# Optimization experiments

Hardware: AMD Instinct MI355X
Metric: run time of the kernel (lower is better)

The kernel has to match this reference:

```python
import jax, jax.numpy as jnp
import numpy as np

N, D, H, C, E = 16384, 768, 768, 2, 20

def setup_inputs() -> dict:
    key = jax.random.key(0)
    k1, k2, k3, k4, k5, k6 = jax.random.split(key, 6)
    return {
        "embeddings": jax.random.normal(k1, (N, D), dtype=jnp.float32),
        "component_idx": jax.random.randint(k2, (N,), 0, E, dtype=jnp.int64),
        "W1": jax.random.normal(k3, (E, D, H), dtype=jnp.float32) * (1.0 / np.sqrt(D)),
        "b1": jnp.zeros((E, H), dtype=jnp.float32),
        "W2": jax.random.normal(k4, (E, H, C), dtype=jnp.float32) * (1.0 / np.sqrt(H)),
        "b2": jnp.zeros((E, C), dtype=jnp.float32),
    }

def reference(embeddings, component_idx, W1, b1, W2, b2):
    # Each token n goes through expert component_idx[n]:
    #   y = relu(x @ W1[e] + b1[e]) @ W2[e] + b2[e]
    # The torch module's mask/cat/argsort reassembly is mathematically a
    # per-token select of its own expert's output at the original position.
    # Dense-expert formulation (standard jax MoE fallback), then gather.
    h = jax.nn.relu(jnp.einsum('nd,edh->enh', embeddings, W1) + b1[:, None, :])  # [E,N,H]
    y = jnp.einsum('enh,ehc->enc', h, W2) + b2[:, None, :]                        # [E,N,C]
    n_idx = jnp.arange(embeddings.shape[0])
    return y[component_idx, n_idx]  # [N,C]
```

## Files before the change

### kernel.cpp

```cpp
#include <hip/hip_runtime.h>

#define N_D 768
#define N_H 768
#define N_C 2
#define N_E 20
#define MT 128
#define NT 128
#define BK 32
#define KT (N_D / BK)
#define ROWB (N_D * 2)
#define SLOTMAX 160

typedef __attribute__((ext_vector_type(8))) short short8;
typedef __attribute__((ext_vector_type(4))) float f32x4;

__device__ __forceinline__ unsigned short f2bf(float f) {
  unsigned u = __builtin_bit_cast(unsigned, f);
  u += 0x7FFFu + ((u >> 16) & 1u);
  return (unsigned short)(u >> 16);
}

#define GLD_LDS16(gp, lp)                                                        \
  __builtin_amdgcn_global_load_lds(                                              \
      (const __attribute__((address_space(1))) void*)(gp),                       \
      (__attribute__((address_space(3))) void*)(lp), 16, 0, 0)


__global__ __launch_bounds__(256) void k_hist(const int* __restrict__ cidx,
                                              int* __restrict__ counts, int n) {
  __shared__ int lc[N_E];
  if (threadIdx.x < N_E) lc[threadIdx.x] = 0;
  __syncthreads();
  for (int i = blockIdx.x * blockDim.x + threadIdx.x; i < n;
       i += gridDim.x * blockDim.x) {
    int e = cidx[i];
    e = e < 0 ? 0 : (e >= N_E ? N_E - 1 : e);
    atomicAdd(&lc[e], 1);
  }
  __syncthreads();
  if (threadIdx.x < N_E) atomicAdd(&counts[threadIdx.x], lc[threadIdx.x]);
}

__global__ __launch_bounds__(64) void k_scan(const int* __restrict__ counts,
                                             int* __restrict__ offsets,
                                             int* __restrict__ cursor,
                                             int* __restrict__ slots) {
  int t = threadIdx.x;
  if (t < N_E) {
    int run = 0;
    for (int e = 0; e < t; ++e) run += counts[e];
    offsets[t] = run;
    cursor[t] = run;
  }
  if (t < 8) {
    int idx = 0;
    for (int e = t; e < N_E; e += 8) {
      int nt = (counts[e] + MT - 1) / MT;
      for (int m = 0; m < nt; ++m)
        for (int bx = 0; bx < 6; ++bx)
          if (idx < SLOTMAX) slots[t * SLOTMAX + idx++] = e | (m << 8) | (bx << 16);
    }
    for (; idx < SLOTMAX; ++idx) slots[t * SLOTMAX + idx] = -1;
  }
}

__global__ __launch_bounds__(256) void k_scatter(const int* __restrict__ cidx,
                                                 int* __restrict__ cursor,
                                                 int* __restrict__ sorted, int n) {
  __shared__ int lc[N_E];
  __shared__ int lbase[N_E];
  int tid = threadIdx.x;
  if (tid < N_E) lc[tid] = 0;
  __syncthreads();
  int i = blockIdx.x * blockDim.x + tid;
  int e = 0, p = 0;
  if (i < n) {
    e = cidx[i];
    e = e < 0 ? 0 : (e >= N_E ? N_E - 1 : e);
    p = atomicAdd(&lc[e], 1);
  }
  __syncthreads();
  if (tid < N_E) lbase[tid] = atomicAdd(&cursor[tid], lc[tid]);
  __syncthreads();
  if (i < n) sorted[lbase[e] + p] = i;
}


__global__ __launch_bounds__(192) void k_gather(const float* __restrict__ emb,
                                                const int* __restrict__ sorted,
                                                unsigned short* __restrict__ Xg,
                                                int n) {
  int row = blockIdx.x;
  int j = threadIdx.x;
  ushort4 o;
  if (row < n) {
    float4 v = ((const float4*)(emb + (size_t)sorted[row] * N_D))[j];
    o.x = f2bf(v.x);
    o.y = f2bf(v.y);
    o.z = f2bf(v.z);
    o.w = f2bf(v.w);
  } else {
    o.x = o.y = o.z = o.w = 0;
  }
  ((ushort4*)(Xg + (size_t)row * N_D))[j] = o;
}


__global__ __launch_bounds__(256) void k_w1_cvt(const float* __restrict__ W1,
                                                unsigned short* __restrict__ W1t) {
  __shared__ float tile[64][65];
  int e = blockIdx.z, h0 = blockIdx.x * 64, d0 = blockIdx.y * 64;
  const float* src = W1 + (size_t)e * N_D * N_H;
  unsigned short* dst = W1t + (size_t)e * N_H * N_D;
  int tx = threadIdx.x & 15, ty = threadIdx.x >> 4;
  for (int s = 0; s < 4; ++s) {
    int d = s * 16 + ty;
    float4 v = *(const float4*)&src[(size_t)(d0 + d) * N_H + h0 + tx * 4];
    tile[d][tx * 4 + 0] = v.x;
    tile[d][tx * 4 + 1] = v.y;
    tile[d][tx * 4 + 2] = v.z;
    tile[d][tx * 4 + 3] = v.w;
  }
  __syncthreads();
  int px = threadIdx.x & 7, py = threadIdx.x >> 3;
  for (int s = 0; s < 2; ++s) {
    int h = s * 32 + py;
    short8 v;
    for (int j = 0; j < 8; ++j)
      v[j] = (short)f2bf(tile[px * 8 + j][h]);
    *(short8*)&dst[(size_t)(h0 + h) * N_D + d0 + px * 8] = v;
  }
}


__global__ __launch_bounds__(256, 4) void k_gemm(
    const unsigned short* __restrict__ Xg, const unsigned short* __restrict__ W1t,
    const float* __restrict__ b1, const float* __restrict__ W2,
    const float* __restrict__ b2, const int* __restrict__ sorted,
    const int* __restrict__ counts, const int* __restrict__ offsets,
    const int* __restrict__ slots, float* __restrict__ out) {
  const int p = blockIdx.x;
  const int sv = slots[(p & 7) * SLOTMAX + (p >> 3)];
  if (sv < 0) return;
  const int e = sv & 255;
  const int m0 = ((sv >> 8) & 255) * MT;
  const int n0 = (sv >> 16) * NT;
  const int off = offsets[e];
  const int cnt_rel = counts[e] - m0;

  __shared__ unsigned short lA[2][MT * BK];
  __shared__ unsigned short lB[2][NT * BK];

  const int tid = threadIdx.x;
  const int wid = tid >> 6, lane = tid & 63;
  const int wm = (wid >> 1) * 64, wn = (wid & 1) * 64;
  const int quad = lane >> 4, lm = lane & 15;

  const int R0 = wid * 32 + lm;
  const char* agp = (const char*)Xg + (size_t)(off + m0 + R0) * ROWB + quad * 16;
  const char* bgp = (const char*)W1t + (size_t)e * N_H * ROWB +
                    (size_t)(n0 + R0) * ROWB + quad * 16;
  unsigned short* lap[2] = {&lA[0][(wid * 32) * BK], &lA[1][(wid * 32) * BK]};
  unsigned short* lbp[2] = {&lB[0][(wid * 32) * BK], &lB[1][(wid * 32) * BK]};

#define ISSUE_BATCH(kk, b)                                                       \
  do {                                                                           \
    const char* a_ = agp + (kk)*64;                                              \
    const char* b_ = bgp + (kk)*64;                                              \
    GLD_LDS16(a_, lap[b]);                                                       \
    GLD_LDS16(a_ + 16 * ROWB, lap[b] + 16 * BK);                                 \
    GLD_LDS16(b_, lbp[b]);                                                       \
    GLD_LDS16(b_ + 16 * ROWB, lbp[b] + 16 * BK);                                 \
  } while (0)

  f32x4 acc[4][4] = {};

  ISSUE_BATCH(0, 0);
  ISSUE_BATCH(1, 1);

  const int fa = quad * 128 + lm * 8;

#define GEMM_BODY(kt, cur, DO_ISSUE)                                             \
  do {                                                                           \
    short8 af[4], bfr[4];                                                        \
    for (int i = 0; i < 4; ++i)                                                  \
      af[i] = *(const short8*)&lA[cur][((wm >> 4) + i) * 512 + fa];              \
    for (int j = 0; j < 4; ++j)                                                  \
      bfr[j] = *(const short8*)&lB[cur][((wn >> 4) + j) * 512 + fa];             \
    asm volatile("s_waitcnt lgkmcnt(0)\n\ts_barrier" ::: "memory");              \
    if (DO_ISSUE) ISSUE_BATCH((kt) + 2, cur);                                    \
    for (int i = 0; i < 4; ++i)                                                  \
      for (int j = 0; j < 4; ++j)                                                \
        acc[i][j] = __builtin_amdgcn_mfma_f32_16x16x32_bf16(af[i], bfr[j],       \
                                                            acc[i][j], 0, 0, 0); \
  } while (0)

#pragma unroll
  for (int kt = 0; kt < KT - 1; ++kt) {
    const int cur = kt & 1;
    asm volatile("s_waitcnt vmcnt(4)\n\ts_barrier" ::: "memory");
    GEMM_BODY(kt, cur, kt < KT - 2);
  }
  {
    asm volatile("s_waitcnt vmcnt(0)\n\ts_barrier" ::: "memory");
    GEMM_BODY(KT - 1, (KT - 1) & 1, false);
  }

  float y0[4][4], y1[4][4];
  for (int i = 0; i < 4; ++i)
    for (int r = 0; r < 4; ++r) y0[i][r] = y1[i][r] = 0.f;

  for (int j = 0; j < 4; ++j) {
    int col = n0 + wn + j * 16 + lm;
    float bias = b1[e * N_H + col];
    float2 w2 = *(const float2*)&W2[((size_t)e * N_H + col) * N_C];
    for (int i = 0; i < 4; ++i) {
      f32x4 a = acc[i][j];
      for (int r = 0; r < 4; ++r) {
        float h = a[r] + bias;
        h = h > 0.f ? h : 0.f;
        y0[i][r] += h * w2.x;
        y1[i][r] += h * w2.y;
      }
    }
  }
  for (int s = 1; s < 16; s <<= 1) {
    for (int i = 0; i < 4; ++i)
      for (int r = 0; r < 4; ++r) {
        y0[i][r] += __shfl_xor(y0[i][r], s, 64);
        y1[i][r] += __shfl_xor(y1[i][r], s, 64);
      }
  }
  if (lm == 0) {
    const bool add_bias = (n0 == 0) && (wn == 0);
    float bb0 = add_bias ? b2[e * N_C + 0] : 0.f;
    float bb1 = add_bias ? b2[e * N_C + 1] : 0.f;
    for (int i = 0; i < 4; ++i) {
      for (int r = 0; r < 4; ++r) {
        int mrel = wm + i * 16 + quad * 4 + r;
        if (mrel < cnt_rel) {
          int token = sorted[off + m0 + mrel];
          atomicAdd(&out[(size_t)token * N_C + 0], y0[i][r] + bb0);
          atomicAdd(&out[(size_t)token * N_C + 1], y1[i][r] + bb1);
        }
      }
    }
  }
}


extern "C" void kernel_launch(void* const* d_in, const int* in_sizes, int n_in,
                              void* d_out, int out_size, void* d_ws, size_t ws_size,
                              hipStream_t stream) {
  const float* emb = (const float*)d_in[0];
  const int* cidx = (const int*)d_in[1];
  const float* W1 = (const float*)d_in[2];
  const float* b1 = (const float*)d_in[3];
  const float* W2 = (const float*)d_in[4];
  const float* b2 = (const float*)d_in[5];
  float* out = (float*)d_out;
  const int n = in_sizes[1];

  char* ws = (char*)d_ws;
  int* counts = (int*)ws;
  int* offsets = (int*)(ws + 128);
  int* cursor = (int*)(ws + 256);
  int* slots = (int*)(ws + 1024);
  int* sorted = (int*)(ws + 8192);
  size_t sorted_bytes = ((size_t)n * 4 + 255) & ~(size_t)255;
  unsigned short* Xg = (unsigned short*)(ws + 8192 + sorted_bytes);
  int pcap = n + MT;
  unsigned short* W1t = Xg + (size_t)pcap * N_D;

  hipMemsetAsync(d_ws, 0, 1024, stream);
  hipMemsetAsync(d_out, 0, (size_t)out_size * sizeof(float), stream);
  int nb = (n + 255) / 256;
  k_hist<<<nb, 256, 0, stream>>>(cidx, counts, n);
  k_scan<<<1, 64, 0, stream>>>(counts, offsets, cursor, slots);
  k_scatter<<<nb, 256, 0, stream>>>(cidx, cursor, sorted, n);
  k_gather<<<pcap, 192, 0, stream>>>(emb, sorted, Xg, n);
  k_w1_cvt<<<dim3(N_H / 64, N_D / 64, N_E), 256, 0, stream>>>(W1, W1t);
  k_gemm<<<8 * SLOTMAX, 256, 0, stream>>>(Xg, W1t, b1, W2, b2, sorted, counts,
                                          offsets, slots, out);
}
```

Measured before the change: 224.6 us.

## Fuse routing prep into one block, merge conversions, restructure GEMM to full-H tiles

The histogram, scan, scatter and output-zeroing launches are merged into a single one-block prep kernel, and the two memsets are dropped. The embedding gather and W1 transpose-convert become one launch. The GEMM now gives each 512-thread block 64 rows and the full hidden width. The whole A tile (64x768) is staged in LDS once, and B fragments are streamed straight from global into registers with prefetch, which removes the per-k-step barriers and the split over six column blocks. This cuts launch overhead and redundant A reloads, at the cost of heavier register use, serialized sorting in one block, and B reads that are not shared through LDS.

```diff
diff --git a/kernel.cpp b/kernel.cpp
--- a/kernel.cpp
+++ b/kernel.cpp
@@ -4,12 +4,10 @@
 #define N_H 768
 #define N_C 2
 #define N_E 20
-#define MT 128
-#define NT 128
-#define BK 32
-#define KT (N_D / BK)
+#define MG 64
+#define KT 24
+#define SLOTMAX 96
 #define ROWB (N_D * 2)
-#define SLOTMAX 160
 
 typedef __attribute__((ext_vector_type(8))) short short8;
 typedef __attribute__((ext_vector_type(4))) float f32x4;
@@ -26,90 +24,91 @@
       (__attribute__((address_space(3))) void*)(lp), 16, 0, 0)
 
 
-__global__ __launch_bounds__(256) void k_hist(const int* __restrict__ cidx,
-                                              int* __restrict__ counts, int n) {
-  __shared__ int lc[N_E];
-  if (threadIdx.x < N_E) lc[threadIdx.x] = 0;
-  __syncthreads();
-  for (int i = blockIdx.x * blockDim.x + threadIdx.x; i < n;
-       i += gridDim.x * blockDim.x) {
-    int e = cidx[i];
-    e = e < 0 ? 0 : (e >= N_E ? N_E - 1 : e);
-    atomicAdd(&lc[e], 1);
-  }
-  __syncthreads();
-  if (threadIdx.x < N_E) atomicAdd(&counts[threadIdx.x], lc[threadIdx.x]);
-}
-
-__global__ __launch_bounds__(64) void k_scan(const int* __restrict__ counts,
-                                             int* __restrict__ offsets,
-                                             int* __restrict__ cursor,
-                                             int* __restrict__ slots) {
-  int t = threadIdx.x;
-  if (t < N_E) {
+__global__ __launch_bounds__(1024) void k_prep(const int* __restrict__ cidx,
+                                               int n, int* __restrict__ counts,
+                                               int* __restrict__ offsets,
+                                               int* __restrict__ slots,
+                                               int* __restrict__ sorted,
+                                               float* __restrict__ out,
+                                               int out_elems) {
+  __shared__ int lcnt[N_E], lbase[N_E], lcur[N_E];
+  const int tid = threadIdx.x;
+  for (int i = tid; i < out_elems; i += 1024) out[i] = 0.f;
+  if (tid < N_E) lcnt[tid] = 0;
+  __syncthreads();
+  const int rounds = (n + 1023) >> 10;
+  for (int r = 0; r < rounds; ++r) {
+    int i = tid + (r << 10);
+    if (i < n) {
+      int e = cidx[i];
+      e = e < 0 ? 0 : (e >= N_E ? N_E - 1 : e);
+      atomicAdd(&lcnt[e], 1);
+    }
+  }
+  __syncthreads();
+  if (tid == 0) {
     int run = 0;
-    for (int e = 0; e < t; ++e) run += counts[e];
-    offsets[t] = run;
-    cursor[t] = run;
-  }
-  if (t < 8) {
-    int idx = 0;
-    for (int e = t; e < N_E; e += 8) {
-      int nt = (counts[e] + MT - 1) / MT;
-      for (int m = 0; m < nt; ++m)
-        for (int bx = 0; bx < 6; ++bx)
-          if (idx < SLOTMAX) slots[t * SLOTMAX + idx++] = e | (m << 8) | (bx << 16);
-    }
-    for (; idx < SLOTMAX; ++idx) slots[t * SLOTMAX + idx] = -1;
-  }
-}
-
-__global__ __launch_bounds__(256) void k_scatter(const int* __restrict__ cidx,
-                                                 int* __restrict__ cursor,
-                                                 int* __restrict__ sorted, int n) {
-  __shared__ int lc[N_E];
-  __shared__ int lbase[N_E];
-  int tid = threadIdx.x;
-  if (tid < N_E) lc[tid] = 0;
-  __syncthreads();
-  int i = blockIdx.x * blockDim.x + tid;
-  int e = 0, p = 0;
-  if (i < n) {
-    e = cidx[i];
-    e = e < 0 ? 0 : (e >= N_E ? N_E - 1 : e);
-    p = atomicAdd(&lc[e], 1);
-  }
-  __syncthreads();
-  if (tid < N_E) lbase[tid] = atomicAdd(&cursor[tid], lc[tid]);
-  __syncthreads();
-  if (i < n) sorted[lbase[e] + p] = i;
-}
-
-
-__global__ __launch_bounds__(192) void k_gather(const float* __restrict__ emb,
-                                                const int* __restrict__ sorted,
-                                                unsigned short* __restrict__ Xg,
-                                                int n) {
-  int row = blockIdx.x;
-  int j = threadIdx.x;
-  ushort4 o;
-  if (row < n) {
-    float4 v = ((const float4*)(emb + (size_t)sorted[row] * N_D))[j];
-    o.x = f2bf(v.x);
-    o.y = f2bf(v.y);
-    o.z = f2bf(v.z);
-    o.w = f2bf(v.w);
-  } else {
-    o.x = o.y = o.z = o.w = 0;
-  }
-  ((ushort4*)(Xg + (size_t)row * N_D))[j] = o;
-}
-
-
-__global__ __launch_bounds__(256) void k_w1_cvt(const float* __restrict__ W1,
-                                                unsigned short* __restrict__ W1t) {
+    for (int e = 0; e < N_E; ++e) {
+      lbase[e] = run;
+      run += lcnt[e];
+    }
+  }
+  __syncthreads();
+  if (tid < N_E) {
+    counts[tid] = lcnt[tid];
+    offsets[tid] = lbase[tid];
+    lcur[tid] = lbase[tid];
+  }
+  if (tid >= 64 && tid < 72) {
+    int x = tid - 64, idx = 0;
+    for (int e = x; e < N_E; e += 8) {
+      int nt = (lcnt[e] + MG - 1) / MG;
+      for (int m = 0; m < nt && idx < SLOTMAX; ++m)
+        slots[x * SLOTMAX + idx++] = e | (m << 8);
+    }
+    for (; idx < SLOTMAX; ++idx) slots[x * SLOTMAX + idx] = -1;
+  }
+  __syncthreads();
+  for (int r = 0; r < rounds; ++r) {
+    int i = tid + (r << 10);
+    if (i < n) {
+      int e = cidx[i];
+      e = e < 0 ? 0 : (e >= N_E ? N_E - 1 : e);
+      int p = atomicAdd(&lcur[e], 1);
+      sorted[p] = i;
+    }
+  }
+}
+
+
+__global__ __launch_bounds__(256) void k_cvt(const float* __restrict__ emb,
+                                             const int* __restrict__ sorted,
+                                             unsigned short* __restrict__ Xg,
+                                             int n, int pcap,
+                                             const float* __restrict__ W1,
+                                             unsigned short* __restrict__ W1t) {
   __shared__ float tile[64][65];
-  int e = blockIdx.z, h0 = blockIdx.x * 64, d0 = blockIdx.y * 64;
+  int b = blockIdx.x;
+  if (b < pcap) {
+    int j = threadIdx.x;
+    if (j < 192) {
+      ushort4 o;
+      if (b < n) {
+        float4 v = ((const float4*)(emb + (size_t)sorted[b] * N_D))[j];
+        o.x = f2bf(v.x);
+        o.y = f2bf(v.y);
+        o.z = f2bf(v.z);
+        o.w = f2bf(v.w);
+      } else {
+        o.x = o.y = o.z = o.w = 0;
+      }
+      ((ushort4*)(Xg + (size_t)b * N_D))[j] = o;
+    }
+    return;
+  }
+  b -= pcap;
+  int e = b / 144, rem = b % 144;
+  int h0 = (rem % 12) * 64, d0 = (rem / 12) * 64;
   const float* src = W1 + (size_t)e * N_D * N_H;
   unsigned short* dst = W1t + (size_t)e * N_H * N_D;
   int tx = threadIdx.x & 15, ty = threadIdx.x >> 4;
@@ -133,89 +132,71 @@
 }
 
 
-__global__ __launch_bounds__(256, 4) void k_gemm(
+__global__ __launch_bounds__(512, 2) void k_gemm(
     const unsigned short* __restrict__ Xg, const unsigned short* __restrict__ W1t,
     const float* __restrict__ b1, const float* __restrict__ W2,
     const float* __restrict__ b2, const int* __restrict__ sorted,
     const int* __restrict__ counts, const int* __restrict__ offsets,
     const int* __restrict__ slots, float* __restrict__ out) {
-  const int p = blockIdx.x;
-  const int sv = slots[(p & 7) * SLOTMAX + (p >> 3)];
+  const int sv = slots[(blockIdx.x & 7) * SLOTMAX + (blockIdx.x >> 3)];
   if (sv < 0) return;
   const int e = sv & 255;
-  const int m0 = ((sv >> 8) & 255) * MT;
-  const int n0 = (sv >> 16) * NT;
+  const int m0 = (sv >> 8) * MG;
   const int off = offsets[e];
   const int cnt_rel = counts[e] - m0;
 
-  __shared__ unsigned short lA[2][MT * BK];
-  __shared__ unsigned short lB[2][NT * BK];
+  __shared__ unsigned short lA[KT * 16 * 128];
 
   const int tid = threadIdx.x;
   const int wid = tid >> 6, lane = tid & 63;
-  const int wm = (wid >> 1) * 64, wn = (wid & 1) * 64;
+  const int rg = wid >> 2;
+  const int cs = wid & 3;
   const int quad = lane >> 4, lm = lane & 15;
 
-  const int R0 = wid * 32 + lm;
-  const char* agp = (const char*)Xg + (size_t)(off + m0 + R0) * ROWB + quad * 16;
-  const char* bgp = (const char*)W1t + (size_t)e * N_H * ROWB +
-                    (size_t)(n0 + R0) * ROWB + quad * 16;
-  unsigned short* lap[2] = {&lA[0][(wid * 32) * BK], &lA[1][(wid * 32) * BK]};
-  unsigned short* lbp[2] = {&lB[0][(wid * 32) * BK], &lB[1][(wid * 32) * BK]};
-
-#define ISSUE_BATCH(kk, b)                                                       \
-  do {                                                                           \
-    const char* a_ = agp + (kk)*64;                                              \
-    const char* b_ = bgp + (kk)*64;                                              \
-    GLD_LDS16(a_, lap[b]);                                                       \
-    GLD_LDS16(a_ + 16 * ROWB, lap[b] + 16 * BK);                                 \
-    GLD_LDS16(b_, lbp[b]);                                                       \
-    GLD_LDS16(b_ + 16 * ROWB, lbp[b] + 16 * BK);                                 \
-  } while (0)
-
-  f32x4 acc[4][4] = {};
-
-  ISSUE_BATCH(0, 0);
-  ISSUE_BATCH(1, 1);
-
-  const int fa = quad * 128 + lm * 8;
-
-#define GEMM_BODY(kt, cur, DO_ISSUE)                                             \
-  do {                                                                           \
-    short8 af[4], bfr[4];                                                        \
-    for (int i = 0; i < 4; ++i)                                                  \
-      af[i] = *(const short8*)&lA[cur][((wm >> 4) + i) * 512 + fa];              \
-    for (int j = 0; j < 4; ++j)                                                  \
-      bfr[j] = *(const short8*)&lB[cur][((wn >> 4) + j) * 512 + fa];             \
-    asm volatile("s_waitcnt lgkmcnt(0)\n\ts_barrier" ::: "memory");              \
-    if (DO_ISSUE) ISSUE_BATCH((kt) + 2, cur);                                    \
-    for (int i = 0; i < 4; ++i)                                                  \
-      for (int j = 0; j < 4; ++j)                                                \
-        acc[i][j] = __builtin_amdgcn_mfma_f32_16x16x32_bf16(af[i], bfr[j],       \
-                                                            acc[i][j], 0, 0, 0); \
-  } while (0)
-
-#pragma unroll
-  for (int kt = 0; kt < KT - 1; ++kt) {
-    const int cur = kt & 1;
-    asm volatile("s_waitcnt vmcnt(4)\n\ts_barrier" ::: "memory");
-    GEMM_BODY(kt, cur, kt < KT - 2);
-  }
-  {
-    asm volatile("s_waitcnt vmcnt(0)\n\ts_barrier" ::: "memory");
-    GEMM_BODY(KT - 1, (KT - 1) & 1, false);
-  }
-
-  float y0[4][4], y1[4][4];
-  for (int i = 0; i < 4; ++i)
+  const char* abase = (const char*)Xg + (size_t)(off + m0) * ROWB;
+  for (int t = 0; t < 12; ++t) {
+    int idx = wid * 12 + t;
+    int kt = idx >> 2, grp = idx & 3;
+    const char* gp = abase + (size_t)(grp * 16 + lm) * ROWB + kt * 64 + quad * 16;
+    GLD_LDS16(gp, (char*)lA + ((size_t)idx << 10));
+  }
+
+  const char* bbase = (const char*)W1t +
+                      ((size_t)e * N_H + cs * 192 + lm) * ROWB + quad * 16;
+  float4 bq[12];
+#pragma unroll
+  for (int ct = 0; ct < 12; ++ct)
+    bq[ct] = *(const float4*)(bbase + ct * 16 * ROWB);
+
+  __syncthreads();
+
+  f32x4 acc[2][12] = {};
+
+#pragma unroll
+  for (int kt = 0; kt < KT; ++kt) {
+    short8 a0 = *(const short8*)&lA[(kt * 16 + (rg * 2 + 0) * 4 + quad) * 128 + lm * 8];
+    short8 a1 = *(const short8*)&lA[(kt * 16 + (rg * 2 + 1) * 4 + quad) * 128 + lm * 8];
+#pragma unroll
+    for (int ct = 0; ct < 12; ++ct) {
+      short8 b = __builtin_bit_cast(short8, bq[ct]);
+      acc[0][ct] = __builtin_amdgcn_mfma_f32_16x16x32_bf16(a0, b, acc[0][ct], 0, 0, 0);
+      acc[1][ct] = __builtin_amdgcn_mfma_f32_16x16x32_bf16(a1, b, acc[1][ct], 0, 0, 0);
+      if (kt < KT - 1)
+        bq[ct] = *(const float4*)(bbase + ct * 16 * ROWB + (kt + 1) * 64);
+    }
+  }
+
+  float y0[2][4], y1[2][4];
+  for (int i = 0; i < 2; ++i)
     for (int r = 0; r < 4; ++r) y0[i][r] = y1[i][r] = 0.f;
 
-  for (int j = 0; j < 4; ++j) {
-    int col = n0 + wn + j * 16 + lm;
+#pragma unroll
+  for (int ct = 0; ct < 12; ++ct) {
+    int col = cs * 192 + ct * 16 + lm;
     float bias = b1[e * N_H + col];
     float2 w2 = *(const float2*)&W2[((size_t)e * N_H + col) * N_C];
-    for (int i = 0; i < 4; ++i) {
-      f32x4 a = acc[i][j];
+    for (int i = 0; i < 2; ++i) {
+      f32x4 a = acc[i][ct];
       for (int r = 0; r < 4; ++r) {
         float h = a[r] + bias;
         h = h > 0.f ? h : 0.f;
@@ -225,19 +206,18 @@
     }
   }
   for (int s = 1; s < 16; s <<= 1) {
-    for (int i = 0; i < 4; ++i)
+    for (int i = 0; i < 2; ++i)
       for (int r = 0; r < 4; ++r) {
         y0[i][r] += __shfl_xor(y0[i][r], s, 64);
         y1[i][r] += __shfl_xor(y1[i][r], s, 64);
       }
   }
   if (lm == 0) {
-    const bool add_bias = (n0 == 0) && (wn == 0);
-    float bb0 = add_bias ? b2[e * N_C + 0] : 0.f;
-    float bb1 = add_bias ? b2[e * N_C + 1] : 0.f;
-    for (int i = 0; i < 4; ++i) {
+    float bb0 = (cs == 0) ? b2[e * N_C + 0] : 0.f;
+    float bb1 = (cs == 0) ? b2[e * N_C + 1] : 0.f;
+    for (int i = 0; i < 2; ++i) {
       for (int r = 0; r < 4; ++r) {
-        int mrel = wm + i * 16 + quad * 4 + r;
+        int mrel = rg * 32 + i * 16 + quad * 4 + r;
         if (mrel < cnt_rel) {
           int token = sorted[off + m0 + mrel];
           atomicAdd(&out[(size_t)token * N_C + 0], y0[i][r] + bb0);
@@ -264,22 +244,16 @@
   char* ws = (char*)d_ws;
   int* counts = (int*)ws;
   int* offsets = (int*)(ws + 128);
-  int* cursor = (int*)(ws + 256);
   int* slots = (int*)(ws + 1024);
   int* sorted = (int*)(ws + 8192);
   size_t sorted_bytes = ((size_t)n * 4 + 255) & ~(size_t)255;
   unsigned short* Xg = (unsigned short*)(ws + 8192 + sorted_bytes);
-  int pcap = n + MT;
+  int pcap = n + MG;
   unsigned short* W1t = Xg + (size_t)pcap * N_D;
 
-  hipMemsetAsync(d_ws, 0, 1024, stream);
-  hipMemsetAsync(d_out, 0, (size_t)out_size * sizeof(float), stream);
-  int nb = (n + 255) / 256;
-  k_hist<<<nb, 256, 0, stream>>>(cidx, counts, n);
-  k_scan<<<1, 64, 0, stream>>>(counts, offsets, cursor, slots);
-  k_scatter<<<nb, 256, 0, stream>>>(cidx, cursor, sorted, n);
-  k_gather<<<pcap, 192, 0, stream>>>(emb, sorted, Xg, n);
-  k_w1_cvt<<<dim3(N_H / 64, N_D / 64, N_E), 256, 0, stream>>>(W1, W1t);
-  k_gemm<<<8 * SLOTMAX, 256, 0, stream>>>(Xg, W1t, b1, W2, b2, sorted, counts,
+  k_prep<<<1, 1024, 0, stream>>>(cidx, n, counts, offsets, slots, sorted, out,
+                                 out_size);
+  k_cvt<<<pcap + N_E * 144, 256, 0, stream>>>(emb, sorted, Xg, n, pcap, W1, W1t);
+  k_gemm<<<8 * SLOTMAX, 512, 0, stream>>>(Xg, W1t, b1, W2, b2, sorted, counts,
                                           offsets, slots, out);
 }
```

Result: slower. 306.8 us (+36.6%).
